# Kernel optimization log

Measured on AMD Instinct MI355X. Metric: run time of the kernel, lower is better.

The kernel has to match this reference:

```python
import jax, jax.numpy as jnp
import numpy as np

N_NODES = 50000
N_EDGES = 600000
D_IN = 128
D_HID = 128


def setup_inputs() -> dict:
    key = jax.random.key(0)
    ks = jax.random.split(key, 6)
    x = jax.random.normal(ks[0], (N_NODES, D_IN), dtype=jnp.float32)
    edge_index = jax.random.randint(ks[1], (2, N_EDGES), 0, N_NODES, dtype=jnp.int64)
    s1 = 1.0 / np.sqrt(D_IN)
    s2 = 1.0 / np.sqrt(D_HID)
    W1_l = jax.random.normal(ks[2], (D_IN, D_HID), dtype=jnp.float32) * s1
    b1 = jnp.zeros((D_HID,), dtype=jnp.float32)
    W1_r = jax.random.normal(ks[3], (D_IN, D_HID), dtype=jnp.float32) * s1
    W2_l = jax.random.normal(ks[4], (D_HID, 1), dtype=jnp.float32) * s2
    b2 = jnp.zeros((1,), dtype=jnp.float32)
    W2_r = jax.random.normal(ks[5], (D_HID, 1), dtype=jnp.float32) * s2
    return {"x": x, "edge_index": edge_index, "W1_l": W1_l, "b1": b1,
            "W1_r": W1_r, "W2_l": W2_l, "b2": b2, "W2_r": W2_r}


def _sage_conv(x, edge_index, W_l, b, W_r):
    # PyG SAGEConv (aggr='mean', root_weight=True):
    #   out = lin_l(mean_{j in N(i)} x_j) + lin_r(x_i)
    n = x.shape[0]
    src, dst = edge_index[0], edge_index[1]
    msg = x[src]                                               # [E, d] gather
    agg = jax.ops.segment_sum(msg, dst, num_segments=n)        # [N, d] scatter-add
    deg = jax.ops.segment_sum(jnp.ones((src.shape[0],), x.dtype), dst,
                              num_segments=n)                  # [N]
    agg = agg / jnp.maximum(deg, 1.0)[:, None]                 # mean (deg>=1 guard)
    return agg @ W_l + b + x @ W_r


def reference(x, edge_index, W1_l, b1, W1_r, W2_l, b2, W2_r):
    h = jax.nn.relu(_sage_conv(x, edge_index, W1_l, b1, W1_r))
    # Dropout(0.2) is identity in eval mode.
    out = _sage_conv(h, edge_index, W2_l, b2, W2_r)            # [N, 1]
    return out.reshape(-1)
```

## Files before the change

kernel.cpp:

```cpp
#include <hip/hip_runtime.h>

#define DIM 128
#define CAP 32
#define NBIN 782
#define SEGB 1024
#define BB 250
#define PER 2400
#define WB 128

typedef __attribute__((ext_vector_type(8))) _Float16 f16x8;
typedef __attribute__((ext_vector_type(4))) _Float16 f16x4;
typedef __attribute__((ext_vector_type(4))) float f32x4;
typedef __attribute__((ext_vector_type(2))) float f32x2;

__global__ __launch_bounds__(256) void k_prep(const float* __restrict__ W1l,
                                              const float* __restrict__ W1r,
                                              _Float16* __restrict__ Wt2,
                                              int* __restrict__ gCur) {
  int bid = blockIdx.x, t = threadIdx.x;
  if (bid < WB) {
    int idx = bid * 256 + t;
    int nn = idx >> 7, k = idx & 127;
    float v = (nn < 128) ? W1l[(size_t)k * 128 + nn]
                         : W1r[(size_t)k * 128 + (nn - 128)];
    Wt2[(size_t)nn * 128 + k] = (_Float16)v;
  } else {
    for (int i = t; i < NBIN; i += 256) gCur[i] = i * SEGB;
  }
}

__global__ __launch_bounds__(256) void k_scatgemm(
    const int* __restrict__ src, const int* __restrict__ dst,
    int* __restrict__ gCur, unsigned int* __restrict__ coarse, int E,
    const float* __restrict__ x, const _Float16* __restrict__ Wt2,
    unsigned char* __restrict__ Y1h, _Float16* __restrict__ Y2h, int n) {
  int bid = blockIdx.x;
  int tid = threadIdx.x;
  if (bid < BB) {
    __shared__ int h[NBIN];
    __shared__ int cur[NBIN];
    for (int i = tid; i < NBIN; i += 256) h[i] = 0;
    __syncthreads();
    const int4* D4 = (const int4*)(dst + bid * PER);
    const int4* S4 = (const int4*)(src + bid * PER);
    int nchunk = PER / 4;
    for (int c = tid; c < nchunk; c += 256) {
      int4 d = D4[c];
      atomicAdd(&h[d.x >> 6], 1);
      atomicAdd(&h[d.y >> 6], 1);
      atomicAdd(&h[d.z >> 6], 1);
      atomicAdd(&h[d.w >> 6], 1);
    }
    __syncthreads();
    for (int b = tid; b < NBIN; b += 256) {
      int c = h[b];
      cur[b] = c ? atomicAdd(&gCur[b], c) : 0;
    }
    __syncthreads();
    for (int c = tid; c < nchunk; c += 256) {
      int4 d = D4[c];
      int4 sv = S4[c];
      int pa = atomicAdd(&cur[d.x >> 6], 1);
      int pb = atomicAdd(&cur[d.y >> 6], 1);
      int pc = atomicAdd(&cur[d.z >> 6], 1);
      int pd = atomicAdd(&cur[d.w >> 6], 1);
      coarse[pa] = ((unsigned int)d.x << 16) | (unsigned int)sv.x;
      coarse[pb] = ((unsigned int)d.y << 16) | (unsigned int)sv.y;
      coarse[pc] = ((unsigned int)d.z << 16) | (unsigned int)sv.z;
      coarse[pd] = ((unsigned int)d.w << 16) | (unsigned int)sv.w;
    }
    return;
  }
  int tile = bid - BB;
  int nb = tile * 64;
  int wv = tid >> 6;
  int lane = tid & 63;
  int q = lane >> 4;
  int l16 = lane & 15;

  __shared__ _Float16 xs[64][136];
  {
#pragma unroll
    for (int it = 0; it < 8; ++it) {
      int slot = it * 256 + tid;
      int row = slot >> 5;
      int c4 = slot & 31;
      int rg = nb + row;
      if (rg > n - 1) rg = n - 1;
      float4 u = *(const float4*)(x + (size_t)rg * 128 + c4 * 4);
      f16x4 hh;
      hh[0] = (_Float16)u.x;
      hh[1] = (_Float16)u.y;
      hh[2] = (_Float16)u.z;
      hh[3] = (_Float16)u.w;
      *(f16x4*)(&xs[row][c4 * 4]) = hh;
    }
  }
  __syncthreads();

  f32x4 acc[4][4];
#pragma unroll
  for (int rt = 0; rt < 4; ++rt)
#pragma unroll
    for (int ct = 0; ct < 4; ++ct) acc[rt][ct] = (f32x4){0.f, 0.f, 0.f, 0.f};

  const _Float16* bp[4];
#pragma unroll
  for (int ct = 0; ct < 4; ++ct)
    bp[ct] = Wt2 + (size_t)(wv * 64 + ct * 16 + l16) * 128;

#pragma unroll
  for (int s = 0; s < 4; ++s) {
    int k0 = s * 32 + q * 8;
    f16x8 a[4], b[4];
#pragma unroll
    for (int rt = 0; rt < 4; ++rt)
      a[rt] = *(const f16x8*)(&xs[rt * 16 + l16][k0]);
#pragma unroll
    for (int ct = 0; ct < 4; ++ct) b[ct] = *(const f16x8*)(bp[ct] + k0);
#pragma unroll
    for (int rt = 0; rt < 4; ++rt)
#pragma unroll
      for (int ct = 0; ct < 4; ++ct)
        acc[rt][ct] = __builtin_amdgcn_mfma_f32_16x16x32_f16(
            a[rt], b[ct], acc[rt][ct], 0, 0, 0);
  }

#pragma unroll
  for (int rt = 0; rt < 4; ++rt) {
#pragma unroll
    for (int r = 0; r < 4; ++r) {
      int row = nb + rt * 16 + q * 4 + r;
      if (row < n) {
        if (wv < 2) {
          unsigned char* yr = Y1h + (size_t)row * 128 + wv * 64 + l16;
#pragma unroll
          for (int ct = 0; ct < 4; ++ct) {
            float v = acc[rt][ct][r];
            int pk = __builtin_amdgcn_cvt_pk_fp8_f32(v, v, 0, false);
            yr[ct * 16] = (unsigned char)(pk & 0xFF);
          }
        } else {
          _Float16* yr = Y2h + (size_t)row * 128 + (wv - 2) * 64 + l16;
#pragma unroll
          for (int ct = 0; ct < 4; ++ct)
            yr[ct * 16] = (_Float16)acc[rt][ct][r];
        }
      }
    }
  }
}

__global__ __launch_bounds__(256) void k_b(const unsigned int* __restrict__ coarse,
                                           const int* __restrict__ gCur,
                                           unsigned short* __restrict__ col,
                                           int* __restrict__ cnt, int n) {
  __shared__ int cur[64];
  int t = threadIdx.x;
  int bin = blockIdx.x;
  if (t < 64) cur[t] = 0;
  __syncthreads();
  int base = bin * SEGB, end = gCur[bin];
  for (int i = base + t; i < end; i += 256) {
    unsigned int rec = coarse[i];
    int d = rec >> 16;
    int s = rec & 0xFFFF;
    int r = atomicAdd(&cur[d & 63], 1);
    if (r < CAP) col[(size_t)d * CAP + r] = (unsigned short)s;
  }
  __syncthreads();
  if (t < 64) {
    int node = bin * 64 + t;
    if (node < n) cnt[node] = cur[t];
  }
}

__device__ __forceinline__ void acc_fp8(float* a, uint2 v) {
  f32x2 p0 = __builtin_amdgcn_cvt_pk_f32_fp8(v.x, false);
  f32x2 p1 = __builtin_amdgcn_cvt_pk_f32_fp8(v.x, true);
  f32x2 p2 = __builtin_amdgcn_cvt_pk_f32_fp8(v.y, false);
  f32x2 p3 = __builtin_amdgcn_cvt_pk_f32_fp8(v.y, true);
  a[0] += p0.x; a[1] += p0.y; a[2] += p1.x; a[3] += p1.y;
  a[4] += p2.x; a[5] += p2.y; a[6] += p3.x; a[7] += p3.y;
}

__global__ __launch_bounds__(256) void k_h(const unsigned char* __restrict__ Y1h,
                                           const _Float16* __restrict__ Y2h,
                                           const int* __restrict__ cnt,
                                           const unsigned short* __restrict__ col,
                                           const float* __restrict__ b1,
                                           const float* __restrict__ w2l,
                                           const float* __restrict__ w2r,
                                           float* __restrict__ sbuf,
                                           float* __restrict__ tbuf, int n) {
  const uint2* Y18 = (const uint2*)Y1h;
  int l16 = threadIdx.x & 15;
  int node = (blockIdx.x * 256 + threadIdx.x) >> 4;
  if (node >= n) return;
  int deg = min(cnt[node], CAP);
  int b = node * CAP, e = b + deg;
  float a[8];
#pragma unroll
  for (int j = 0; j < 8; ++j) a[j] = 0.f;
  int i = b;
  for (; i + 4 <= e; i += 4) {
    uint2 v0 = Y18[(size_t)col[i] * 16 + l16];
    uint2 v1 = Y18[(size_t)col[i + 1] * 16 + l16];
    uint2 v2 = Y18[(size_t)col[i + 2] * 16 + l16];
    uint2 v3 = Y18[(size_t)col[i + 3] * 16 + l16];
    acc_fp8(a, v0);
    acc_fp8(a, v1);
    acc_fp8(a, v2);
    acc_fp8(a, v3);
  }
  for (; i < e; ++i) acc_fp8(a, Y18[(size_t)col[i] * 16 + l16]);
  float inv = 1.0f / (float)max(deg, 1);
  f16x8 y2 = *(const f16x8*)(Y2h + (size_t)node * 128 + l16 * 8);
  float4 bl = *(const float4*)(b1 + l16 * 8);
  float4 bh = *(const float4*)(b1 + l16 * 8 + 4);
  float4 ll = *(const float4*)(w2l + l16 * 8);
  float4 lh = *(const float4*)(w2l + l16 * 8 + 4);
  float4 rl = *(const float4*)(w2r + l16 * 8);
  float4 rh = *(const float4*)(w2r + l16 * 8 + 4);
  float bb[8] = {bl.x, bl.y, bl.z, bl.w, bh.x, bh.y, bh.z, bh.w};
  float wl[8] = {ll.x, ll.y, ll.z, ll.w, lh.x, lh.y, lh.z, lh.w};
  float wr[8] = {rl.x, rl.y, rl.z, rl.w, rh.x, rh.y, rh.z, rh.w};
  float sp = 0.f, tp = 0.f;
#pragma unroll
  for (int j = 0; j < 8; ++j) {
    float h = fmaxf(a[j] * inv + (float)y2[j] + bb[j], 0.f);
    sp += h * wl[j];
    tp += h * wr[j];
  }
#pragma unroll
  for (int m = 1; m < 16; m <<= 1) {
    sp += __shfl_xor(sp, m, 64);
    tp += __shfl_xor(tp, m, 64);
  }
  if (l16 == 0) {
    sbuf[node] = sp;
    tbuf[node] = tp;
  }
}

__global__ __launch_bounds__(256) void k_out(const float* __restrict__ s,
                                             const int* __restrict__ cnt,
                                             const unsigned short* __restrict__ col,
                                             const float* __restrict__ t,
                                             const float* __restrict__ b2,
                                             float* __restrict__ out, int n) {
  int l = threadIdx.x & 15;
  int node = (blockIdx.x * 256 + threadIdx.x) >> 4;
  if (node >= n) return;
  int deg = min(cnt[node], CAP);
  int b = node * CAP;
  float p = 0.f;
  for (int j = l; j < deg; j += 16) p += s[col[b + j]];
#pragma unroll
  for (int m = 1; m < 16; m <<= 1) p += __shfl_xor(p, m, 64);
  if (l == 0)
    out[node] = p / (float)max(deg, 1) + b2[0] + t[node];
}


extern "C" void kernel_launch(void* const* d_in, const int* in_sizes, int n_in,
                              void* d_out, int out_size, void* d_ws,
                              size_t ws_size, hipStream_t stream) {
  const float* x   = (const float*)d_in[0];
  const int*   ei  = (const int*)d_in[1];
  const float* W1l = (const float*)d_in[2];
  const float* b1  = (const float*)d_in[3];
  const float* W1r = (const float*)d_in[4];
  const float* w2l = (const float*)d_in[5];
  const float* b2  = (const float*)d_in[6];
  const float* w2r = (const float*)d_in[7];
  float* out = (float*)d_out;

  int n = in_sizes[0] / DIM;
  int E = in_sizes[1] / 2;
  const int* src = ei;
  const int* dst = ei + E;

  char* ws = (char*)d_ws;
  size_t off = 0;
  auto take = [&](size_t bytes) -> void* {
    void* p = ws + off;
    off = (off + bytes + 511) & ~(size_t)511;
    return p;
  };
  int*            gCur   = (int*)take((size_t)NBIN * 4);
  unsigned int*   coarse = (unsigned int*)take((size_t)NBIN * SEGB * 4);
  int*            cnt    = (int*)take((size_t)n * 4);
  unsigned short* col    = (unsigned short*)take((size_t)n * CAP * 2);
  _Float16*       Wt2    = (_Float16*)take((size_t)256 * 128 * 2);
  unsigned char*  Y1h    = (unsigned char*)take((size_t)n * 128);
  _Float16*       Y2h    = (_Float16*)take((size_t)n * 128 * 2);
  float*          sbuf   = (float*)take((size_t)n * 4);
  float*          tbuf   = (float*)take((size_t)n * 4);
  (void)ws_size; (void)n_in; (void)out_size;

  int gb = (n + 63) / 64;
  int hb = (n * 16 + 255) / 256;

  k_prep<<<WB + 1, 256, 0, stream>>>(W1l, W1r, Wt2, gCur);
  k_scatgemm<<<BB + gb, 256, 0, stream>>>(src, dst, gCur, coarse, E, x, Wt2,
                                          Y1h, Y2h, n);
  k_b<<<NBIN, 256, 0, stream>>>(coarse, gCur, col, cnt, n);
  k_h<<<hb, 256, 0, stream>>>(Y1h, Y2h, cnt, col, b1, w2l, w2r, sbuf, tbuf, n);
  k_out<<<hb, 256, 0, stream>>>(sbuf, cnt, col, tbuf, b2, out, n);
}
```

Measured before the change: 132.9 us.

## Fuse scatter, GEMM, binning, hidden and output stages into one persistent kernel

Merges four kernel launches into one persistent kernel sized from occupancy. Blocks loop over work units and are separated by software grid barriers, and bin-sorting units spin-wait on a counter until all scatter units finish. This removes launch gaps and the tail idle time between stages. In exchange it adds spin-wait and barrier cost, relies on every block being co-resident to avoid deadlock, and may lower occupancy for the gather phases.

```diff
diff --git a/kernel.cpp b/kernel.cpp
--- a/kernel.cpp
+++ b/kernel.cpp
@@ -16,7 +16,8 @@
 __global__ __launch_bounds__(256) void k_prep(const float* __restrict__ W1l,
                                               const float* __restrict__ W1r,
                                               _Float16* __restrict__ Wt2,
-                                              int* __restrict__ gCur) {
+                                              int* __restrict__ gCur,
+                                              int* __restrict__ bars) {
   int bid = blockIdx.x, t = threadIdx.x;
   if (bid < WB) {
     int idx = bid * 256 + t;
@@ -26,240 +27,286 @@
     Wt2[(size_t)nn * 128 + k] = (_Float16)v;
   } else {
     for (int i = t; i < NBIN; i += 256) gCur[i] = i * SEGB;
+    if (t < 8) bars[t] = 0;
   }
 }
 
-__global__ __launch_bounds__(256) void k_scatgemm(
+__device__ __forceinline__ void gridbar(int* cnt, int nblk) {
+  __syncthreads();
+  if (threadIdx.x == 0) {
+    __threadfence();
+    atomicAdd(cnt, 1);
+    while (__hip_atomic_load(cnt, __ATOMIC_RELAXED, __HIP_MEMORY_SCOPE_AGENT) <
+           nblk)
+      __builtin_amdgcn_s_sleep(2);
+  }
+  __syncthreads();
+  __threadfence();
+}
+
+__global__ __launch_bounds__(256, 4) void k_all(
     const int* __restrict__ src, const int* __restrict__ dst,
-    int* __restrict__ gCur, unsigned int* __restrict__ coarse, int E,
+    int* __restrict__ gCur, unsigned int* __restrict__ coarse,
     const float* __restrict__ x, const _Float16* __restrict__ Wt2,
-    unsigned char* __restrict__ Y1h, _Float16* __restrict__ Y2h, int n) {
-  int bid = blockIdx.x;
+    unsigned char* __restrict__ Y1h, _Float16* __restrict__ Y2h,
+    unsigned short* __restrict__ col, int* __restrict__ cnt,
+    const float* __restrict__ b1, const float* __restrict__ w2l,
+    const float* __restrict__ w2r, const float* __restrict__ b2,
+    float* __restrict__ sbuf, float* __restrict__ tbuf,
+    float* __restrict__ out, int* __restrict__ bars, int n, int E) {
+  __shared__ __align__(16) char smem[64 * 136 * 2];
   int tid = threadIdx.x;
-  if (bid < BB) {
-    __shared__ int h[NBIN];
-    __shared__ int cur[NBIN];
-    for (int i = tid; i < NBIN; i += 256) h[i] = 0;
+  int nblk = gridDim.x;
+  int* scat_done = bars + 0;
+  int* bar1 = bars + 1;
+  int* bar2 = bars + 2;
+  const int GB = (n + 63) / 64;
+  const int P1U = BB + GB;
+  const int P1T = P1U + NBIN;
+  const int HU = (n * 16 + 255) / 256;
+
+  for (int u = blockIdx.x; u < P1T; u += nblk) {
     __syncthreads();
-    const int4* D4 = (const int4*)(dst + bid * PER);
-    const int4* S4 = (const int4*)(src + bid * PER);
-    int nchunk = PER / 4;
-    for (int c = tid; c < nchunk; c += 256) {
-      int4 d = D4[c];
-      atomicAdd(&h[d.x >> 6], 1);
-      atomicAdd(&h[d.y >> 6], 1);
-      atomicAdd(&h[d.z >> 6], 1);
-      atomicAdd(&h[d.w >> 6], 1);
+    if (u < BB) {
+      int* h = (int*)smem;
+      int* cur = ((int*)smem) + NBIN;
+      for (int i = tid; i < NBIN; i += 256) h[i] = 0;
+      __syncthreads();
+      const int4* D4 = (const int4*)(dst + u * PER);
+      const int4* S4 = (const int4*)(src + u * PER);
+      int nchunk = PER / 4;
+      for (int c = tid; c < nchunk; c += 256) {
+        int4 d = D4[c];
+        atomicAdd(&h[d.x >> 6], 1);
+        atomicAdd(&h[d.y >> 6], 1);
+        atomicAdd(&h[d.z >> 6], 1);
+        atomicAdd(&h[d.w >> 6], 1);
+      }
+      __syncthreads();
+      for (int b = tid; b < NBIN; b += 256) {
+        int c = h[b];
+        cur[b] = c ? atomicAdd(&gCur[b], c) : 0;
+      }
+      __syncthreads();
+      for (int c = tid; c < nchunk; c += 256) {
+        int4 d = D4[c];
+        int4 sv = S4[c];
+        int pa = atomicAdd(&cur[d.x >> 6], 1);
+        int pb = atomicAdd(&cur[d.y >> 6], 1);
+        int pc = atomicAdd(&cur[d.z >> 6], 1);
+        int pd = atomicAdd(&cur[d.w >> 6], 1);
+        coarse[pa] = ((unsigned int)d.x << 16) | (unsigned int)sv.x;
+        coarse[pb] = ((unsigned int)d.y << 16) | (unsigned int)sv.y;
+        coarse[pc] = ((unsigned int)d.z << 16) | (unsigned int)sv.z;
+        coarse[pd] = ((unsigned int)d.w << 16) | (unsigned int)sv.w;
+      }
+      __syncthreads();
+      if (tid == 0) {
+        __threadfence();
+        atomicAdd(scat_done, 1);
+      }
+    } else if (u < P1U) {
+      int nb = (u - BB) * 64;
+      int wv = tid >> 6;
+      int lane = tid & 63;
+      int q = lane >> 4;
+      int l16 = lane & 15;
+      _Float16(*xs)[136] = (_Float16(*)[136])smem;
+#pragma unroll
+      for (int it = 0; it < 8; ++it) {
+        int slot = it * 256 + tid;
+        int row = slot >> 5;
+        int c4 = slot & 31;
+        int rg = nb + row;
+        if (rg > n - 1) rg = n - 1;
+        float4 uu = *(const float4*)(x + (size_t)rg * 128 + c4 * 4);
+        f16x4 hh;
+        hh[0] = (_Float16)uu.x;
+        hh[1] = (_Float16)uu.y;
+        hh[2] = (_Float16)uu.z;
+        hh[3] = (_Float16)uu.w;
+        *(f16x4*)(&xs[row][c4 * 4]) = hh;
+      }
+      __syncthreads();
+      f32x4 acc[4][4];
+#pragma unroll
+      for (int rt = 0; rt < 4; ++rt)
+#pragma unroll
+        for (int ct = 0; ct < 4; ++ct)
+          acc[rt][ct] = (f32x4){0.f, 0.f, 0.f, 0.f};
+      const _Float16* bp[4];
+#pragma unroll
+      for (int ct = 0; ct < 4; ++ct)
+        bp[ct] = Wt2 + (size_t)(wv * 64 + ct * 16 + l16) * 128;
+#pragma unroll
+      for (int s = 0; s < 4; ++s) {
+        int k0 = s * 32 + q * 8;
+        f16x8 a[4], b[4];
+#pragma unroll
+        for (int rt = 0; rt < 4; ++rt)
+          a[rt] = *(const f16x8*)(&xs[rt * 16 + l16][k0]);
+#pragma unroll
+        for (int ct = 0; ct < 4; ++ct) b[ct] = *(const f16x8*)(bp[ct] + k0);
+#pragma unroll
+        for (int rt = 0; rt < 4; ++rt)
+#pragma unroll
+          for (int ct = 0; ct < 4; ++ct)
+            acc[rt][ct] = __builtin_amdgcn_mfma_f32_16x16x32_f16(
+                a[rt], b[ct], acc[rt][ct], 0, 0, 0);
+      }
+#pragma unroll
+      for (int rt = 0; rt < 4; ++rt) {
+#pragma unroll
+        for (int r = 0; r < 4; ++r) {
+          int row = nb + rt * 16 + q * 4 + r;
+          if (row < n) {
+            if (wv < 2) {
+              unsigned char* yr = Y1h + (size_t)row * 128 + wv * 64 + l16;
+#pragma unroll
+              for (int ct = 0; ct < 4; ++ct) {
+                float v = acc[rt][ct][r];
+                int pk = __builtin_amdgcn_cvt_pk_fp8_f32(v, v, 0, false);
+                yr[ct * 16] = (unsigned char)(pk & 0xFF);
+              }
+            } else {
+              _Float16* yr = Y2h + (size_t)row * 128 + (wv - 2) * 64 + l16;
+#pragma unroll
+              for (int ct = 0; ct < 4; ++ct)
+                yr[ct * 16] = (_Float16)acc[rt][ct][r];
+            }
+          }
+        }
+      }
+    } else {
+      if (tid == 0) {
+        while (__hip_atomic_load(scat_done, __ATOMIC_RELAXED,
+                                 __HIP_MEMORY_SCOPE_AGENT) < BB)
+          __builtin_amdgcn_s_sleep(2);
+      }
+      __syncthreads();
+      __threadfence();
+      int bin = u - P1U;
+      int* cb = (int*)smem;
+      if (tid < 64) cb[tid] = 0;
+      __syncthreads();
+      int base = bin * SEGB, end = gCur[bin];
+      for (int i = base + tid; i < end; i += 256) {
+        unsigned int rec = coarse[i];
+        int d = rec >> 16;
+        int s = rec & 0xFFFF;
+        int r = atomicAdd(&cb[d & 63], 1);
+        if (r < CAP) col[(size_t)d * CAP + r] = (unsigned short)s;
+      }
+      __syncthreads();
+      if (tid < 64) {
+        int node = bin * 64 + tid;
+        if (node < n) cnt[node] = cb[tid];
+      }
     }
-    __syncthreads();
-    for (int b = tid; b < NBIN; b += 256) {
-      int c = h[b];
-      cur[b] = c ? atomicAdd(&gCur[b], c) : 0;
+  }
+
+  gridbar(bar1, nblk);
+
+  {
+    const uint2* Y18 = (const uint2*)Y1h;
+    int l16 = tid & 15;
+    float4 bl = *(const float4*)(b1 + l16 * 8);
+    float4 bh = *(const float4*)(b1 + l16 * 8 + 4);
+    float4 ll = *(const float4*)(w2l + l16 * 8);
+    float4 lh = *(const float4*)(w2l + l16 * 8 + 4);
+    float4 rl = *(const float4*)(w2r + l16 * 8);
+    float4 rh = *(const float4*)(w2r + l16 * 8 + 4);
+    float bb[8] = {bl.x, bl.y, bl.z, bl.w, bh.x, bh.y, bh.z, bh.w};
+    float wl[8] = {ll.x, ll.y, ll.z, ll.w, lh.x, lh.y, lh.z, lh.w};
+    float wr[8] = {rl.x, rl.y, rl.z, rl.w, rh.x, rh.y, rh.z, rh.w};
+    for (int u = blockIdx.x; u < HU; u += nblk) {
+      int node = u * 16 + (tid >> 4);
+      if (node >= n) continue;
+      int deg = min(cnt[node], CAP);
+      int b = node * CAP, e = b + deg;
+      float a[8];
+#pragma unroll
+      for (int j = 0; j < 8; ++j) a[j] = 0.f;
+      int i = b;
+      for (; i + 4 <= e; i += 4) {
+        uint2 v0 = Y18[(size_t)col[i] * 16 + l16];
+        uint2 v1 = Y18[(size_t)col[i + 1] * 16 + l16];
+        uint2 v2 = Y18[(size_t)col[i + 2] * 16 + l16];
+        uint2 v3 = Y18[(size_t)col[i + 3] * 16 + l16];
+        {
+          f32x2 p0 = __builtin_amdgcn_cvt_pk_f32_fp8(v0.x, false);
+          f32x2 p1 = __builtin_amdgcn_cvt_pk_f32_fp8(v0.x, true);
+          f32x2 p2 = __builtin_amdgcn_cvt_pk_f32_fp8(v0.y, false);
+          f32x2 p3 = __builtin_amdgcn_cvt_pk_f32_fp8(v0.y, true);
+          a[0] += p0.x; a[1] += p0.y; a[2] += p1.x; a[3] += p1.y;
+          a[4] += p2.x; a[5] += p2.y; a[6] += p3.x; a[7] += p3.y;
+          p0 = __builtin_amdgcn_cvt_pk_f32_fp8(v1.x, false);
+          p1 = __builtin_amdgcn_cvt_pk_f32_fp8(v1.x, true);
+          p2 = __builtin_amdgcn_cvt_pk_f32_fp8(v1.y, false);
+          p3 = __builtin_amdgcn_cvt_pk_f32_fp8(v1.y, true);
+          a[0] += p0.x; a[1] += p0.y; a[2] += p1.x; a[3] += p1.y;
+          a[4] += p2.x; a[5] += p2.y; a[6] += p3.x; a[7] += p3.y;
+          p0 = __builtin_amdgcn_cvt_pk_f32_fp8(v2.x, false);
+          p1 = __builtin_amdgcn_cvt_pk_f32_fp8(v2.x, true);
+          p2 = __builtin_amdgcn_cvt_pk_f32_fp8(v2.y, false);
+          p3 = __builtin_amdgcn_cvt_pk_f32_fp8(v2.y, true);
+          a[0] += p0.x; a[1] += p0.y; a[2] += p1.x; a[3] += p1.y;
+          a[4] += p2.x; a[5] += p2.y; a[6] += p3.x; a[7] += p3.y;
+          p0 = __builtin_amdgcn_cvt_pk_f32_fp8(v3.x, false);
+          p1 = __builtin_amdgcn_cvt_pk_f32_fp8(v3.x, true);
+          p2 = __builtin_amdgcn_cvt_pk_f32_fp8(v3.y, false);
+          p3 = __builtin_amdgcn_cvt_pk_f32_fp8(v3.y, true);
+          a[0] += p0.x; a[1] += p0.y; a[2] += p1.x; a[3] += p1.y;
+          a[4] += p2.x; a[5] += p2.y; a[6] += p3.x; a[7] += p3.y;
+        }
+      }
+      for (; i < e; ++i) {
+        uint2 v = Y18[(size_t)col[i] * 16 + l16];
+        f32x2 p0 = __builtin_amdgcn_cvt_pk_f32_fp8(v.x, false);
+        f32x2 p1 = __builtin_amdgcn_cvt_pk_f32_fp8(v.x, true);
+        f32x2 p2 = __builtin_amdgcn_cvt_pk_f32_fp8(v.y, false);
+        f32x2 p3 = __builtin_amdgcn_cvt_pk_f32_fp8(v.y, true);
+        a[0] += p0.x; a[1] += p0.y; a[2] += p1.x; a[3] += p1.y;
+        a[4] += p2.x; a[5] += p2.y; a[6] += p3.x; a[7] += p3.y;
+      }
+      float inv = 1.0f / (float)max(deg, 1);
+      f16x8 y2 = *(const f16x8*)(Y2h + (size_t)node * 128 + l16 * 8);
+      float sp = 0.f, tp = 0.f;
+#pragma unroll
+      for (int j = 0; j < 8; ++j) {
+        float hh = fmaxf(a[j] * inv + (float)y2[j] + bb[j], 0.f);
+        sp += hh * wl[j];
+        tp += hh * wr[j];
+      }
+#pragma unroll
+      for (int m = 1; m < 16; m <<= 1) {
+        sp += __shfl_xor(sp, m, 64);
+        tp += __shfl_xor(tp, m, 64);
+      }
+      if (l16 == 0) {
+        sbuf[node] = sp;
+        tbuf[node] = tp;
+      }
     }
-    __syncthreads();
-    for (int c = tid; c < nchunk; c += 256) {
-      int4 d = D4[c];
-      int4 sv = S4[c];
-      int pa = atomicAdd(&cur[d.x >> 6], 1);
-      int pb = atomicAdd(&cur[d.y >> 6], 1);
-      int pc = atomicAdd(&cur[d.z >> 6], 1);
-      int pd = atomicAdd(&cur[d.w >> 6], 1);
-      coarse[pa] = ((unsigned int)d.x << 16) | (unsigned int)sv.x;
-      coarse[pb] = ((unsigned int)d.y << 16) | (unsigned int)sv.y;
-      coarse[pc] = ((unsigned int)d.z << 16) | (unsigned int)sv.z;
-      coarse[pd] = ((unsigned int)d.w << 16) | (unsigned int)sv.w;
+  }
+
+  gridbar(bar2, nblk);
+
+  {
+    int l = tid & 15;
+    float b2v = b2[0];
+    for (int u = blockIdx.x; u < HU; u += nblk) {
+      int node = u * 16 + (tid >> 4);
+      if (node >= n) continue;
+      int deg = min(cnt[node], CAP);
+      int b = node * CAP;
+      float p = 0.f;
+      for (int j = l; j < deg; j += 16) p += sbuf[col[b + j]];
+#pragma unroll
+      for (int m = 1; m < 16; m <<= 1) p += __shfl_xor(p, m, 64);
+      if (l == 0) out[node] = p / (float)max(deg, 1) + b2v + tbuf[node];
     }
-    return;
-  }
-  int tile = bid - BB;
-  int nb = tile * 64;
-  int wv = tid >> 6;
-  int lane = tid & 63;
-  int q = lane >> 4;
-  int l16 = lane & 15;
-
-  __shared__ _Float16 xs[64][136];
-  {
-#pragma unroll
-    for (int it = 0; it < 8; ++it) {
-      int slot = it * 256 + tid;
-      int row = slot >> 5;
-      int c4 = slot & 31;
-      int rg = nb + row;
-      if (rg > n - 1) rg = n - 1;
-      float4 u = *(const float4*)(x + (size_t)rg * 128 + c4 * 4);
-      f16x4 hh;
-      hh[0] = (_Float16)u.x;
-      hh[1] = (_Float16)u.y;
-      hh[2] = (_Float16)u.z;
-      hh[3] = (_Float16)u.w;
-      *(f16x4*)(&xs[row][c4 * 4]) = hh;
-    }
-  }
-  __syncthreads();
-
-  f32x4 acc[4][4];
-#pragma unroll
-  for (int rt = 0; rt < 4; ++rt)
-#pragma unroll
-    for (int ct = 0; ct < 4; ++ct) acc[rt][ct] = (f32x4){0.f, 0.f, 0.f, 0.f};
-
-  const _Float16* bp[4];
-#pragma unroll
-  for (int ct = 0; ct < 4; ++ct)
-    bp[ct] = Wt2 + (size_t)(wv * 64 + ct * 16 + l16) * 128;
-
-#pragma unroll
-  for (int s = 0; s < 4; ++s) {
-    int k0 = s * 32 + q * 8;
-    f16x8 a[4], b[4];
-#pragma unroll
-    for (int rt = 0; rt < 4; ++rt)
-      a[rt] = *(const f16x8*)(&xs[rt * 16 + l16][k0]);
-#pragma unroll
-    for (int ct = 0; ct < 4; ++ct) b[ct] = *(const f16x8*)(bp[ct] + k0);
-#pragma unroll
-    for (int rt = 0; rt < 4; ++rt)
-#pragma unroll
-      for (int ct = 0; ct < 4; ++ct)
-        acc[rt][ct] = __builtin_amdgcn_mfma_f32_16x16x32_f16(
-            a[rt], b[ct], acc[rt][ct], 0, 0, 0);
-  }
-
-#pragma unroll
-  for (int rt = 0; rt < 4; ++rt) {
-#pragma unroll
-    for (int r = 0; r < 4; ++r) {
-      int row = nb + rt * 16 + q * 4 + r;
-      if (row < n) {
-        if (wv < 2) {
-          unsigned char* yr = Y1h + (size_t)row * 128 + wv * 64 + l16;
-#pragma unroll
-          for (int ct = 0; ct < 4; ++ct) {
-            float v = acc[rt][ct][r];
-            int pk = __builtin_amdgcn_cvt_pk_fp8_f32(v, v, 0, false);
-            yr[ct * 16] = (unsigned char)(pk & 0xFF);
-          }
-        } else {
-          _Float16* yr = Y2h + (size_t)row * 128 + (wv - 2) * 64 + l16;
-#pragma unroll
-          for (int ct = 0; ct < 4; ++ct)
-            yr[ct * 16] = (_Float16)acc[rt][ct][r];
-        }
-      }
-    }
-  }
-}
-
-__global__ __launch_bounds__(256) void k_b(const unsigned int* __restrict__ coarse,
-                                           const int* __restrict__ gCur,
-                                           unsigned short* __restrict__ col,
-                                           int* __restrict__ cnt, int n) {
-  __shared__ int cur[64];
-  int t = threadIdx.x;
-  int bin = blockIdx.x;
-  if (t < 64) cur[t] = 0;
-  __syncthreads();
-  int base = bin * SEGB, end = gCur[bin];
-  for (int i = base + t; i < end; i += 256) {
-    unsigned int rec = coarse[i];
-    int d = rec >> 16;
-    int s = rec & 0xFFFF;
-    int r = atomicAdd(&cur[d & 63], 1);
-    if (r < CAP) col[(size_t)d * CAP + r] = (unsigned short)s;
-  }
-  __syncthreads();
-  if (t < 64) {
-    int node = bin * 64 + t;
-    if (node < n) cnt[node] = cur[t];
-  }
-}
-
-__device__ __forceinline__ void acc_fp8(float* a, uint2 v) {
-  f32x2 p0 = __builtin_amdgcn_cvt_pk_f32_fp8(v.x, false);
-  f32x2 p1 = __builtin_amdgcn_cvt_pk_f32_fp8(v.x, true);
-  f32x2 p2 = __builtin_amdgcn_cvt_pk_f32_fp8(v.y, false);
-  f32x2 p3 = __builtin_amdgcn_cvt_pk_f32_fp8(v.y, true);
-  a[0] += p0.x; a[1] += p0.y; a[2] += p1.x; a[3] += p1.y;
-  a[4] += p2.x; a[5] += p2.y; a[6] += p3.x; a[7] += p3.y;
-}
-
-__global__ __launch_bounds__(256) void k_h(const unsigned char* __restrict__ Y1h,
-                                           const _Float16* __restrict__ Y2h,
-                                           const int* __restrict__ cnt,
-                                           const unsigned short* __restrict__ col,
-                                           const float* __restrict__ b1,
-                                           const float* __restrict__ w2l,
-                                           const float* __restrict__ w2r,
-                                           float* __restrict__ sbuf,
-                                           float* __restrict__ tbuf, int n) {
-  const uint2* Y18 = (const uint2*)Y1h;
-  int l16 = threadIdx.x & 15;
-  int node = (blockIdx.x * 256 + threadIdx.x) >> 4;
-  if (node >= n) return;
-  int deg = min(cnt[node], CAP);
-  int b = node * CAP, e = b + deg;
-  float a[8];
-#pragma unroll
-  for (int j = 0; j < 8; ++j) a[j] = 0.f;
-  int i = b;
-  for (; i + 4 <= e; i += 4) {
-    uint2 v0 = Y18[(size_t)col[i] * 16 + l16];
-    uint2 v1 = Y18[(size_t)col[i + 1] * 16 + l16];
-    uint2 v2 = Y18[(size_t)col[i + 2] * 16 + l16];
-    uint2 v3 = Y18[(size_t)col[i + 3] * 16 + l16];
-    acc_fp8(a, v0);
-    acc_fp8(a, v1);
-    acc_fp8(a, v2);
-    acc_fp8(a, v3);
-  }
-  for (; i < e; ++i) acc_fp8(a, Y18[(size_t)col[i] * 16 + l16]);
-  float inv = 1.0f / (float)max(deg, 1);
-  f16x8 y2 = *(const f16x8*)(Y2h + (size_t)node * 128 + l16 * 8);
-  float4 bl = *(const float4*)(b1 + l16 * 8);
-  float4 bh = *(const float4*)(b1 + l16 * 8 + 4);
-  float4 ll = *(const float4*)(w2l + l16 * 8);
-  float4 lh = *(const float4*)(w2l + l16 * 8 + 4);
-  float4 rl = *(const float4*)(w2r + l16 * 8);
-  float4 rh = *(const float4*)(w2r + l16 * 8 + 4);
-  float bb[8] = {bl.x, bl.y, bl.z, bl.w, bh.x, bh.y, bh.z, bh.w};
-  float wl[8] = {ll.x, ll.y, ll.z, ll.w, lh.x, lh.y, lh.z, lh.w};
-  float wr[8] = {rl.x, rl.y, rl.z, rl.w, rh.x, rh.y, rh.z, rh.w};
-  float sp = 0.f, tp = 0.f;
-#pragma unroll
-  for (int j = 0; j < 8; ++j) {
-    float h = fmaxf(a[j] * inv + (float)y2[j] + bb[j], 0.f);
-    sp += h * wl[j];
-    tp += h * wr[j];
-  }
-#pragma unroll
-  for (int m = 1; m < 16; m <<= 1) {
-    sp += __shfl_xor(sp, m, 64);
-    tp += __shfl_xor(tp, m, 64);
-  }
-  if (l16 == 0) {
-    sbuf[node] = sp;
-    tbuf[node] = tp;
-  }
-}
-
-__global__ __launch_bounds__(256) void k_out(const float* __restrict__ s,
-                                             const int* __restrict__ cnt,
-                                             const unsigned short* __restrict__ col,
-                                             const float* __restrict__ t,
-                                             const float* __restrict__ b2,
-                                             float* __restrict__ out, int n) {
-  int l = threadIdx.x & 15;
-  int node = (blockIdx.x * 256 + threadIdx.x) >> 4;
-  if (node >= n) return;
-  int deg = min(cnt[node], CAP);
-  int b = node * CAP;
-  float p = 0.f;
-  for (int j = l; j < deg; j += 16) p += s[col[b + j]];
-#pragma unroll
-  for (int m = 1; m < 16; m <<= 1) p += __shfl_xor(p, m, 64);
-  if (l == 0)
-    out[node] = p / (float)max(deg, 1) + b2[0] + t[node];
+  }
 }
 
 
@@ -289,6 +336,7 @@
     return p;
   };
   int*            gCur   = (int*)take((size_t)NBIN * 4);
+  int*            bars   = (int*)take((size_t)8 * 4);
   unsigned int*   coarse = (unsigned int*)take((size_t)NBIN * SEGB * 4);
   int*            cnt    = (int*)take((size_t)n * 4);
   unsigned short* col    = (unsigned short*)take((size_t)n * CAP * 2);
@@ -299,13 +347,18 @@
   float*          tbuf   = (float*)take((size_t)n * 4);
   (void)ws_size; (void)n_in; (void)out_size;
 
-  int gb = (n + 63) / 64;
-  int hb = (n * 16 + 255) / 256;
-
-  k_prep<<<WB + 1, 256, 0, stream>>>(W1l, W1r, Wt2, gCur);
-  k_scatgemm<<<BB + gb, 256, 0, stream>>>(src, dst, gCur, coarse, E, x, Wt2,
-                                          Y1h, Y2h, n);
-  k_b<<<NBIN, 256, 0, stream>>>(coarse, gCur, col, cnt, n);
-  k_h<<<hb, 256, 0, stream>>>(Y1h, Y2h, cnt, col, b1, w2l, w2r, sbuf, tbuf, n);
-  k_out<<<hb, 256, 0, stream>>>(sbuf, cnt, col, tbuf, b2, out, n);
+  static int gblocks = 0;
+  if (gblocks == 0) {
+    int nb = 0;
+    hipError_t err =
+        hipOccupancyMaxActiveBlocksPerMultiprocessor(&nb, k_all, 256, 0);
+    if (err != hipSuccess || nb < 1) nb = 1;
+    if (nb > 6) nb = 6;
+    gblocks = nb * 256;
+  }
+
+  k_prep<<<WB + 1, 256, 0, stream>>>(W1l, W1r, Wt2, gCur, bars);
+  k_all<<<gblocks, 256, 0, stream>>>(src, dst, gCur, coarse, x, Wt2, Y1h, Y2h,
+                                     col, cnt, b1, w2l, w2r, b2, sbuf, tbuf,
+                                     out, bars, n, E);
 }
```

After: 451.1 us. +239.4%, slower.
